# Kernel tuning notes

Hardware: AMD Instinct MI355X
Metric: run time of the kernel (lower is better)

Reference implementation:

```python
import jax, jax.numpy as jnp
import numpy as np

MEM_DIM = 2048
BATCH = 4096


def setup_inputs() -> dict:
    key = jax.random.key(0)
    ks = jax.random.split(key, 8)
    D = MEM_DIM
    scale = 1.0 / np.sqrt(D)  # torch nn.Linear default init range ~ U(-1/sqrt(D), 1/sqrt(D))
    lc = jax.random.normal(ks[0], (BATCH, D), dtype=jnp.float32)
    lh = jax.random.normal(ks[1], (BATCH, D), dtype=jnp.float32)
    rc = jax.random.normal(ks[2], (BATCH, D), dtype=jnp.float32)
    rh = jax.random.normal(ks[3], (BATCH, D), dtype=jnp.float32)
    # Fused params: columns [0:D]=input gate, [D:2D]=left forget, [2D:3D]=right forget, [3D:4D]=update
    Wl = jax.random.uniform(ks[4], (D, 4 * D), dtype=jnp.float32, minval=-scale, maxval=scale)
    Wr = jax.random.uniform(ks[5], (D, 4 * D), dtype=jnp.float32, minval=-scale, maxval=scale)
    bl = jax.random.uniform(ks[6], (4 * D,), dtype=jnp.float32, minval=-scale, maxval=scale)
    br = jax.random.uniform(ks[7], (4 * D,), dtype=jnp.float32, minval=-scale, maxval=scale)
    return {"lc": lc, "lh": lh, "rc": rc, "rh": rh, "Wl": Wl, "bl": bl, "Wr": Wr, "br": br}


def reference(lc, lh, rc, rh, Wl, bl, Wr, br):
    D = lh.shape[-1]
    # Two fused GEMMs replace 8 separate mem_dim x mem_dim linears (same math).
    g = jnp.dot(lh, Wl) + bl + jnp.dot(rh, Wr) + br  # [B, 4D]
    i = jax.nn.sigmoid(g[:, 0 * D:1 * D])   # input gate
    lf = jax.nn.sigmoid(g[:, 1 * D:2 * D])  # left forget gate
    rf = jax.nn.sigmoid(g[:, 2 * D:3 * D])  # right forget gate
    u = jnp.tanh(g[:, 3 * D:4 * D])         # cell update
    c = i * u + lf * lc + rf * rc
    h = jnp.tanh(c)
    return (c, h)
```

## Files before the change

kernel.cpp:

```cpp
#include <hip/hip_runtime.h>
#include <stdint.h>

#define D_MEM 2048
#define BATCH 4096
#define K_DIM 4096
#define N_DIM 8192

typedef __bf16 bf16x8 __attribute__((ext_vector_type(8)));
typedef float f32x4 __attribute__((ext_vector_type(4)));

typedef const void __attribute__((address_space(1)))* gas_t;
typedef void __attribute__((address_space(3)))* las_t;

__device__ __forceinline__ ushort f2b(float f) {
  union { float f; uint32_t u; } v; v.f = f;
  uint32_t u = v.u + 0x7fffu + ((v.u >> 16) & 1u);
  return (ushort)(u >> 16);
}
__device__ __forceinline__ float b2f(ushort s) {
  union { uint32_t u; float f; } v; v.u = ((uint32_t)s) << 16;
  return v.f;
}
__device__ __forceinline__ float sigm(float x) {
  return 1.0f / (1.0f + __expf(-x));
}
__device__ __forceinline__ float tanh_fast(float x) {
  return __builtin_fmaf(2.0f, sigm(2.0f * x), -1.0f);
}

__global__ void cast_concat_kernel(const float* __restrict__ lh,
                                   const float* __restrict__ rh,
                                   ushort* __restrict__ A) {
  int i4 = blockIdx.x * 256 + threadIdx.x;
  int row = i4 >> 10;
  int col = (i4 & 1023) * 4;
  const float* src = (col < D_MEM) ? (lh + (size_t)row * D_MEM + col)
                                   : (rh + (size_t)row * D_MEM + (col - D_MEM));
  float4 v = *(const float4*)src;
  ushort4 o; o.x = f2b(v.x); o.y = f2b(v.y); o.z = f2b(v.z); o.w = f2b(v.w);
  *(ushort4*)(A + (size_t)row * K_DIM + col) = o;
}

__global__ void transpose_cast_kernel(const float* __restrict__ Wl,
                                      const float* __restrict__ Wr,
                                      ushort* __restrict__ Bt) {
  __shared__ float t[64 * 65];
  const float* W = blockIdx.z ? Wr : Wl;
  int n0 = blockIdx.x * 64;
  int k0 = blockIdx.y * 64;
  int tid = threadIdx.x;
#pragma unroll
  for (int i = 0; i < 4; ++i) {
    int idx = i * 256 + tid;
    int rr = idx >> 4;
    int c4 = (idx & 15) * 4;
    float4 v = *(const float4*)(W + (size_t)(k0 + rr) * N_DIM + n0 + c4);
    t[rr * 65 + c4 + 0] = v.x;
    t[rr * 65 + c4 + 1] = v.y;
    t[rr * 65 + c4 + 2] = v.z;
    t[rr * 65 + c4 + 3] = v.w;
  }
  __syncthreads();
  int kbase = (blockIdx.z ? D_MEM : 0) + k0;
#pragma unroll
  for (int i = 0; i < 4; ++i) {
    int idx = i * 256 + tid;
    int rr = idx >> 4;
    int c4 = (idx & 15) * 4;
    ushort4 o;
    o.x = f2b(t[(c4 + 0) * 65 + rr]);
    o.y = f2b(t[(c4 + 1) * 65 + rr]);
    o.z = f2b(t[(c4 + 2) * 65 + rr]);
    o.w = f2b(t[(c4 + 3) * 65 + rr]);
    *(ushort4*)(Bt + (size_t)(n0 + rr) * K_DIM + kbase + c4) = o;
  }
}

__device__ __forceinline__ void stage2(const ushort* g0, const ushort* g1,
                                       char* dst, int wave) {
  __builtin_amdgcn_global_load_lds((gas_t)g0, (las_t)(dst + wave * 1024), 16, 0, 0);
  __builtin_amdgcn_global_load_lds((gas_t)g1, (las_t)(dst + 8192 + wave * 1024), 16, 0, 0);
}

#define HALF(KS, BUF, GA0, GA1, DSTA, GB0, GB1, DSTB)                          \
  do {                                                                         \
    stage2((GA0), (GA1), (DSTA), wave);                                        \
    stage2((GB0), (GB1), (DSTB), wave);                                        \
    bf16x8 af0[4], af1[4], bq[4];                                              \
    const char* ab_ = AsB + (BUF)*32768 + (KS)*16384;                          \
    const char* bb_ = BsB + (BUF)*32768 + (KS)*16384;                          \
    _Pragma("unroll") for (int f_ = 0; f_ < 4; ++f_)                           \
        af0[f_] = *(const bf16x8*)(ab_ + aoff[0][f_]);                         \
    _Pragma("unroll") for (int j_ = 0; j_ < 4; ++j_)                           \
        bq[j_] = *(const bf16x8*)(bb_ + boff[j_]);                             \
    _Pragma("unroll") for (int f_ = 0; f_ < 4; ++f_)                           \
        af1[f_] = *(const bf16x8*)(ab_ + aoff[1][f_]);                         \
    __builtin_amdgcn_s_setprio(1);                                             \
    _Pragma("unroll") for (int i_ = 0; i_ < 4; ++i_)                           \
        _Pragma("unroll") for (int j_ = 0; j_ < 4; ++j_)                       \
            acc[i_][j_] = __builtin_amdgcn_mfma_f32_16x16x32_bf16(             \
                af0[i_], bq[j_], acc[i_][j_], 0, 0, 0);                        \
    _Pragma("unroll") for (int i_ = 0; i_ < 4; ++i_)                           \
        _Pragma("unroll") for (int j_ = 0; j_ < 4; ++j_)                       \
            acc[4 + i_][j_] = __builtin_amdgcn_mfma_f32_16x16x32_bf16(         \
                af1[i_], bq[j_], acc[4 + i_][j_], 0, 0, 0);                    \
    __builtin_amdgcn_s_setprio(0);                                             \
    asm volatile("s_waitcnt vmcnt(8)" ::: "memory");                           \
    __builtin_amdgcn_s_barrier();                                              \
  } while (0)

__global__ __launch_bounds__(512, 2) void gemm_bf16_kernel(
    const ushort* __restrict__ A,
    const ushort* __restrict__ B,
    ushort* __restrict__ C) {
  __shared__ char smem[131072];
  char* AsB = smem;
  char* BsB = smem + 65536;
  const int K = K_DIM, N = N_DIM;

  int tid = threadIdx.x;
  int lane = tid & 63, wave = tid >> 6;
  int wm = wave >> 2, wn = wave & 3;
  int q = lane >> 4, r = lane & 15;

  int bid = blockIdx.x;
  int swz = (bid & 7) * 64 + (bid >> 3);
  int m0 = (swz >> 5) * 256;
  int n0 = (swz & 31) * 256;

  int ci0 = tid, ci1 = 512 + tid;
  int r0 = ci0 >> 2, c0 = (ci0 & 3) ^ ((r0 ^ (r0 >> 2)) & 3);
  int r1 = ci1 >> 2, c1 = (ci1 & 3) ^ ((r1 ^ (r1 >> 2)) & 3);
  const ushort* sA0 = A + (size_t)(m0 + r0) * K + c0 * 8;
  const ushort* sA1 = A + (size_t)(m0 + r1) * K + c1 * 8;
  const ushort* sB0 = B + (size_t)(n0 + r0) * K + c0 * 8;
  const ushort* sB1 = B + (size_t)(n0 + r1) * K + c1 * 8;

  int swzr = (r ^ (r >> 2)) & 3;
  int aoff[2][4], boff[4];
#pragma unroll
  for (int mh = 0; mh < 2; ++mh)
#pragma unroll
    for (int f = 0; f < 4; ++f) {
      int row = wm * 128 + mh * 64 + f * 16 + r;
      aoff[mh][f] = row * 64 + (q ^ swzr) * 16;
    }
#pragma unroll
  for (int j = 0; j < 4; ++j) {
    int col = wn * 64 + j * 16 + r;
    boff[j] = col * 64 + (q ^ swzr) * 16;
  }

  f32x4 acc[8][4];
#pragma unroll
  for (int i = 0; i < 8; ++i)
#pragma unroll
    for (int j = 0; j < 4; ++j) acc[i][j] = f32x4{0.f, 0.f, 0.f, 0.f};

  stage2(sA0,      sA1,      AsB + 0,     wave);
  stage2(sB0,      sB1,      BsB + 0,     wave);
  stage2(sA0 + 32, sA1 + 32, AsB + 16384, wave);
  stage2(sB0 + 32, sB1 + 32, BsB + 16384, wave);
  stage2(sA0 + 64, sA1 + 64, AsB + 32768, wave);
  stage2(sB0 + 64, sB1 + 64, BsB + 32768, wave);
  asm volatile("s_waitcnt vmcnt(8)" ::: "memory");
  __builtin_amdgcn_s_barrier();

#pragma unroll 1
  for (int t = 0; t < 64; t += 2) {
    const int o1 = (t + 1) * 64;
    const int o2 = (t + 2 < 64 ? t + 2 : 63) * 64;
    const int o3 = (t + 3 < 64 ? t + 3 : 63) * 64;
    HALF(0, 0, sA0 + o1 + 32, sA1 + o1 + 32, AsB + 49152,
               sB0 + o1 + 32, sB1 + o1 + 32, BsB + 49152);
    HALF(1, 0, sA0 + o2,      sA1 + o2,      AsB + 0,
               sB0 + o2,      sB1 + o2,      BsB + 0);
    HALF(0, 1, sA0 + o2 + 32, sA1 + o2 + 32, AsB + 16384,
               sB0 + o2 + 32, sB1 + o2 + 32, BsB + 16384);
    HALF(1, 1, sA0 + o3,      sA1 + o3,      AsB + 32768,
               sB0 + o3,      sB1 + o3,      BsB + 32768);
  }

#pragma unroll
  for (int i = 0; i < 8; ++i) {
    int gm_base = m0 + wm * 128 + i * 16 + q * 4;
#pragma unroll
    for (int j = 0; j < 4; ++j) {
      int gn = n0 + wn * 64 + j * 16 + r;
      size_t base = (size_t)gm_base * N + gn;
#pragma unroll
      for (int e = 0; e < 4; ++e)
        C[base + (size_t)e * N] = f2b(acc[i][j][e]);
    }
  }
}

__global__ void gate_kernel(const ushort* __restrict__ G,
                            const float* __restrict__ bl,
                            const float* __restrict__ br,
                            const float* __restrict__ lc,
                            const float* __restrict__ rc,
                            float* __restrict__ out) {
  int i4 = blockIdx.x * 256 + threadIdx.x;
  int row = i4 >> 9;
  int col = (i4 & 511) * 4;
  size_t gbase = (size_t)row * N_DIM + col;

  ushort4 ui = *(const ushort4*)(G + gbase);
  ushort4 uf = *(const ushort4*)(G + gbase + 1 * D_MEM);
  ushort4 ug = *(const ushort4*)(G + gbase + 2 * D_MEM);
  ushort4 uu = *(const ushort4*)(G + gbase + 3 * D_MEM);

  float4 bli = *(const float4*)(bl + col);
  float4 blf = *(const float4*)(bl + col + 1 * D_MEM);
  float4 blr = *(const float4*)(bl + col + 2 * D_MEM);
  float4 blu = *(const float4*)(bl + col + 3 * D_MEM);
  float4 bri = *(const float4*)(br + col);
  float4 brf = *(const float4*)(br + col + 1 * D_MEM);
  float4 brr = *(const float4*)(br + col + 2 * D_MEM);
  float4 bru = *(const float4*)(br + col + 3 * D_MEM);

  float4 vlc = *(const float4*)(lc + (size_t)row * D_MEM + col);
  float4 vrc = *(const float4*)(rc + (size_t)row * D_MEM + col);

  float4 vc, vh;
  {
    float gi = b2f(ui.x) + bli.x + bri.x;
    float gf = b2f(uf.x) + blf.x + brf.x;
    float gr = b2f(ug.x) + blr.x + brr.x;
    float gu = b2f(uu.x) + blu.x + bru.x;
    vc.x = sigm(gi) * tanh_fast(gu) + sigm(gf) * vlc.x + sigm(gr) * vrc.x;
    vh.x = tanh_fast(vc.x);
  }
  {
    float gi = b2f(ui.y) + bli.y + bri.y;
    float gf = b2f(uf.y) + blf.y + brf.y;
    float gr = b2f(ug.y) + blr.y + brr.y;
    float gu = b2f(uu.y) + blu.y + bru.y;
    vc.y = sigm(gi) * tanh_fast(gu) + sigm(gf) * vlc.y + sigm(gr) * vrc.y;
    vh.y = tanh_fast(vc.y);
  }
  {
    float gi = b2f(ui.z) + bli.z + bri.z;
    float gf = b2f(uf.z) + blf.z + brf.z;
    float gr = b2f(ug.z) + blr.z + brr.z;
    float gu = b2f(uu.z) + blu.z + bru.z;
    vc.z = sigm(gi) * tanh_fast(gu) + sigm(gf) * vlc.z + sigm(gr) * vrc.z;
    vh.z = tanh_fast(vc.z);
  }
  {
    float gi = b2f(ui.w) + bli.w + bri.w;
    float gf = b2f(uf.w) + blf.w + brf.w;
    float gr = b2f(ug.w) + blr.w + brr.w;
    float gu = b2f(uu.w) + blu.w + bru.w;
    vc.w = sigm(gi) * tanh_fast(gu) + sigm(gf) * vlc.w + sigm(gr) * vrc.w;
    vh.w = tanh_fast(vc.w);
  }

  size_t obase = (size_t)row * D_MEM + col;
  *(float4*)(out + obase) = vc;
  *(float4*)(out + (size_t)BATCH * D_MEM + obase) = vh;
}

extern "C" void kernel_launch(void* const* d_in, const int* in_sizes, int n_in,
                              void* d_out, int out_size, void* d_ws, size_t ws_size,
                              hipStream_t stream) {
  const float* lc = (const float*)d_in[0];
  const float* lh = (const float*)d_in[1];
  const float* rc = (const float*)d_in[2];
  const float* rh = (const float*)d_in[3];
  const float* Wl = (const float*)d_in[4];
  const float* bl = (const float*)d_in[5];
  const float* Wr = (const float*)d_in[6];
  const float* br = (const float*)d_in[7];
  float* out = (float*)d_out;

  char* ws = (char*)d_ws;
  ushort* A  = (ushort*)ws;
  ushort* Bt = (ushort*)(ws + (size_t)32 * 1024 * 1024);
  ushort* G  = (ushort*)(ws + (size_t)96 * 1024 * 1024);

  cast_concat_kernel<<<16384, 256, 0, stream>>>(lh, rh, A);
  dim3 tg(128, 32, 2);
  transpose_cast_kernel<<<tg, 256, 0, stream>>>(Wl, Wr, Bt);
  gemm_bf16_kernel<<<512, 512, 0, stream>>>(A, Bt, G);
  gate_kernel<<<8192, 256, 0, stream>>>(G, bl, br, lc, rc, out);
}
```

Measured before the change: 540.8 us.

## Fuse LSTM gate epilogue into GEMM by interleaving gate columns per tile

Each GEMM block's N-tile now gathers 64 hidden columns from each of the four gate slices, so one thread holds the i, f, r and u pre-activations for the same hidden unit. The gate math, bias add, lc/rc reads and c/h writes move into the GEMM epilogue, which removes the bf16 G intermediate and the separate gate kernel launch. The cost is that the epilogue's lc/rc loads and output stores are now scalar rather than vectorized, and the pre-activations are no longer rounded to bf16 before the gates.

Result: no change. 535.9 us (-0.9%).

```diff
diff --git a/kernel.cpp b/kernel.cpp
--- a/kernel.cpp
+++ b/kernel.cpp
@@ -112,11 +112,15 @@
 __global__ __launch_bounds__(512, 2) void gemm_bf16_kernel(
     const ushort* __restrict__ A,
     const ushort* __restrict__ B,
-    ushort* __restrict__ C) {
+    const float* __restrict__ bl,
+    const float* __restrict__ br,
+    const float* __restrict__ lc,
+    const float* __restrict__ rc,
+    float* __restrict__ out) {
   __shared__ char smem[131072];
   char* AsB = smem;
   char* BsB = smem + 65536;
-  const int K = K_DIM, N = N_DIM;
+  const int K = K_DIM;
 
   int tid = threadIdx.x;
   int lane = tid & 63, wave = tid >> 6;
@@ -126,15 +130,17 @@
   int bid = blockIdx.x;
   int swz = (bid & 7) * 64 + (bid >> 3);
   int m0 = (swz >> 5) * 256;
-  int n0 = (swz & 31) * 256;
+  int d0 = (swz & 31) * 64;
 
   int ci0 = tid, ci1 = 512 + tid;
   int r0 = ci0 >> 2, c0 = (ci0 & 3) ^ ((r0 ^ (r0 >> 2)) & 3);
   int r1 = ci1 >> 2, c1 = (ci1 & 3) ^ ((r1 ^ (r1 >> 2)) & 3);
+  int nb0 = (r0 >> 6) * D_MEM + d0 + (r0 & 63);
+  int nb1 = (r1 >> 6) * D_MEM + d0 + (r1 & 63);
   const ushort* sA0 = A + (size_t)(m0 + r0) * K + c0 * 8;
   const ushort* sA1 = A + (size_t)(m0 + r1) * K + c1 * 8;
-  const ushort* sB0 = B + (size_t)(n0 + r0) * K + c0 * 8;
-  const ushort* sB1 = B + (size_t)(n0 + r1) * K + c1 * 8;
+  const ushort* sB0 = B + (size_t)nb0 * K + c0 * 8;
+  const ushort* sB1 = B + (size_t)nb1 * K + c1 * 8;
 
   int swzr = (r ^ (r >> 2)) & 3;
   int aoff[2][4], boff[4];
@@ -147,8 +153,8 @@
     }
 #pragma unroll
   for (int j = 0; j < 4; ++j) {
-    int col = wn * 64 + j * 16 + r;
-    boff[j] = col * 64 + (q ^ swzr) * 16;
+    int row = j * 64 + wn * 16 + r;
+    boff[j] = row * 64 + (q ^ swzr) * 16;
   }
 
   f32x4 acc[8][4];
@@ -181,85 +187,30 @@
                sB0 + o3,      sB1 + o3,      BsB + 32768);
   }
 
+  int d = d0 + wn * 16 + r;
+  float bs0 = bl[0 * D_MEM + d] + br[0 * D_MEM + d];
+  float bs1 = bl[1 * D_MEM + d] + br[1 * D_MEM + d];
+  float bs2 = bl[2 * D_MEM + d] + br[2 * D_MEM + d];
+  float bs3 = bl[3 * D_MEM + d] + br[3 * D_MEM + d];
+  float* outc = out + d;
+  float* outh = out + (size_t)BATCH * D_MEM + d;
+
 #pragma unroll
   for (int i = 0; i < 8; ++i) {
-    int gm_base = m0 + wm * 128 + i * 16 + q * 4;
-#pragma unroll
-    for (int j = 0; j < 4; ++j) {
-      int gn = n0 + wn * 64 + j * 16 + r;
-      size_t base = (size_t)gm_base * N + gn;
-#pragma unroll
-      for (int e = 0; e < 4; ++e)
-        C[base + (size_t)e * N] = f2b(acc[i][j][e]);
+    int mb = m0 + wm * 128 + i * 16 + q * 4;
+#pragma unroll
+    for (int e = 0; e < 4; ++e) {
+      size_t mrow = (size_t)(mb + e) * D_MEM;
+      float gi = acc[i][0][e] + bs0;
+      float gf = acc[i][1][e] + bs1;
+      float gr = acc[i][2][e] + bs2;
+      float gu = acc[i][3][e] + bs3;
+      float c = sigm(gi) * tanh_fast(gu) + sigm(gf) * lc[mrow + d] +
+                sigm(gr) * rc[mrow + d];
+      outc[mrow] = c;
+      outh[mrow] = tanh_fast(c);
     }
   }
-}
-
-__global__ void gate_kernel(const ushort* __restrict__ G,
-                            const float* __restrict__ bl,
-                            const float* __restrict__ br,
-                            const float* __restrict__ lc,
-                            const float* __restrict__ rc,
-                            float* __restrict__ out) {
-  int i4 = blockIdx.x * 256 + threadIdx.x;
-  int row = i4 >> 9;
-  int col = (i4 & 511) * 4;
-  size_t gbase = (size_t)row * N_DIM + col;
-
-  ushort4 ui = *(const ushort4*)(G + gbase);
-  ushort4 uf = *(const ushort4*)(G + gbase + 1 * D_MEM);
-  ushort4 ug = *(const ushort4*)(G + gbase + 2 * D_MEM);
-  ushort4 uu = *(const ushort4*)(G + gbase + 3 * D_MEM);
-
-  float4 bli = *(const float4*)(bl + col);
-  float4 blf = *(const float4*)(bl + col + 1 * D_MEM);
-  float4 blr = *(const float4*)(bl + col + 2 * D_MEM);
-  float4 blu = *(const float4*)(bl + col + 3 * D_MEM);
-  float4 bri = *(const float4*)(br + col);
-  float4 brf = *(const float4*)(br + col + 1 * D_MEM);
-  float4 brr = *(const float4*)(br + col + 2 * D_MEM);
-  float4 bru = *(const float4*)(br + col + 3 * D_MEM);
-
-  float4 vlc = *(const float4*)(lc + (size_t)row * D_MEM + col);
-  float4 vrc = *(const float4*)(rc + (size_t)row * D_MEM + col);
-
-  float4 vc, vh;
-  {
-    float gi = b2f(ui.x) + bli.x + bri.x;
-    float gf = b2f(uf.x) + blf.x + brf.x;
-    float gr = b2f(ug.x) + blr.x + brr.x;
-    float gu = b2f(uu.x) + blu.x + bru.x;
-    vc.x = sigm(gi) * tanh_fast(gu) + sigm(gf) * vlc.x + sigm(gr) * vrc.x;
-    vh.x = tanh_fast(vc.x);
-  }
-  {
-    float gi = b2f(ui.y) + bli.y + bri.y;
-    float gf = b2f(uf.y) + blf.y + brf.y;
-    float gr = b2f(ug.y) + blr.y + brr.y;
-    float gu = b2f(uu.y) + blu.y + bru.y;
-    vc.y = sigm(gi) * tanh_fast(gu) + sigm(gf) * vlc.y + sigm(gr) * vrc.y;
-    vh.y = tanh_fast(vc.y);
-  }
-  {
-    float gi = b2f(ui.z) + bli.z + bri.z;
-    float gf = b2f(uf.z) + blf.z + brf.z;
-    float gr = b2f(ug.z) + blr.z + brr.z;
-    float gu = b2f(uu.z) + blu.z + bru.z;
-    vc.z = sigm(gi) * tanh_fast(gu) + sigm(gf) * vlc.z + sigm(gr) * vrc.z;
-    vh.z = tanh_fast(vc.z);
-  }
-  {
-    float gi = b2f(ui.w) + bli.w + bri.w;
-    float gf = b2f(uf.w) + blf.w + brf.w;
-    float gr = b2f(ug.w) + blr.w + brr.w;
-    float gu = b2f(uu.w) + blu.w + bru.w;
-    vc.w = sigm(gi) * tanh_fast(gu) + sigm(gf) * vlc.w + sigm(gr) * vrc.w;
-    vh.w = tanh_fast(vc.w);
-  }
-
-  size_t obase = (size_t)row * D_MEM + col;
-  *(float4*)(out + obase) = vc;
-  *(float4*)(out + (size_t)BATCH * D_MEM + obase) = vh;
 }
 
 extern "C" void kernel_launch(void* const* d_in, const int* in_sizes, int n_in,
@@ -278,11 +229,9 @@
   char* ws = (char*)d_ws;
   ushort* A  = (ushort*)ws;
   ushort* Bt = (ushort*)(ws + (size_t)32 * 1024 * 1024);
-  ushort* G  = (ushort*)(ws + (size_t)96 * 1024 * 1024);
 
   cast_concat_kernel<<<16384, 256, 0, stream>>>(lh, rh, A);
   dim3 tg(128, 32, 2);
   transpose_cast_kernel<<<tg, 256, 0, stream>>>(Wl, Wr, Bt);
-  gemm_bf16_kernel<<<512, 512, 0, stream>>>(A, Bt, G);
-  gate_kernel<<<8192, 256, 0, stream>>>(G, bl, br, lc, rc, out);
-}
+  gemm_bf16_kernel<<<512, 512, 0, stream>>>(A, Bt, bl, br, lc, rc, out);
+}
```
